# Kernel optimization log

Measured on AMD Instinct MI355X. Metric: run time of the kernel, lower is better.

Reference implementation:

```python
import jax, jax.numpy as jnp
import numpy as np

NC, K, SD = 8, 1024, 64
L = NC * SD
B = 8192
TAU = 0.07
COMMIT_W = 1.0
CONTRAST_W = 1.0
EPS = 1e-12


def setup_inputs() -> dict:
    key = jax.random.key(0)
    kz, ke = jax.random.split(key)
    z = jax.random.normal(kz, (B, L), dtype=jnp.float32)
    embeddings = jax.random.normal(ke, (NC, K, SD), dtype=jnp.float32)
    return {"z": z, "embeddings": embeddings}


def reference(z, embeddings):
    sg = jax.lax.stop_gradient
    Bn, Ln = z.shape
    nc, k, sd = embeddings.shape
    zr = z.reshape(Bn, nc, sd)  # (B, nc, sd)

    # squared distances via ||z||^2 - 2 z.e + ||e||^2 -> (B, nc, K), avoids (B,nc,K,sd)
    z2 = jnp.sum(zr * zr, axis=-1)[:, :, None]
    e2 = jnp.sum(embeddings * embeddings, axis=-1)[None, :, :]
    cross = jnp.einsum('bnd,nkd->bnk', zr, embeddings)
    dists = z2 - 2.0 * cross + e2
    indices = jnp.argmin(dists, axis=-1)  # (B, nc)

    # codebook gather
    quant_splits = embeddings[jnp.arange(nc)[None, :], indices]  # (B, nc, sd)
    quant_z = quant_splits.reshape(Bn, Ln)

    commit_loss = jnp.mean((sg(quant_z) - z) ** 2)
    embed_loss = jnp.mean((quant_z - sg(z)) ** 2)
    total_commit = commit_loss + embed_loss

    quant_z_st = z + sg(quant_z - z)

    z_norm = z / jnp.maximum(jnp.linalg.norm(z, axis=-1, keepdims=True), EPS)
    q_det = sg(quant_z)
    q_norm = q_det / jnp.maximum(jnp.linalg.norm(q_det, axis=-1, keepdims=True), EPS)
    logits = jnp.matmul(q_norm, z_norm.T) / TAU  # (B, B)
    # cross-entropy with labels = arange(B)
    contrastive = jnp.mean(jax.nn.logsumexp(logits, axis=1) - jnp.diagonal(logits))

    return (quant_z_st, COMMIT_W * total_commit, CONTRAST_W * contrastive, indices)
```

## Files before the change

kernel.cpp:

```cpp
#include <hip/hip_runtime.h>
#include <cstdint>
#include <cstddef>

#define NCB   8
#define KC    1024
#define SDIM  64
#define LDIM  512
#define BATCH 8192
#define INV_TAU (1.0f/0.07f)
#define K2E  20.60992915555662f
#define DBIAS 256.0f

typedef __bf16 bf16_t;
typedef bf16_t bf16x8 __attribute__((ext_vector_type(8)));
typedef float  floatx4 __attribute__((ext_vector_type(4)));
typedef int    intx8  __attribute__((ext_vector_type(8)));
typedef unsigned int u32;

__device__ __forceinline__ unsigned short f2bf(float f) {
    union { float f; unsigned int u; } c; c.f = f;
    unsigned int u = c.u;
    u += 0x7fffu + ((u >> 16) & 1u);
    return (unsigned short)(u >> 16);
}
__device__ __forceinline__ float bf2f(unsigned short h) {
    union { unsigned int u; float f; } c; c.u = ((unsigned int)h) << 16;
    return c.f;
}
__device__ __forceinline__ float exp2_fast(float x) {
    float r; asm("v_exp_f32 %0, %1" : "=v"(r) : "v"(x)); return r;
}
__device__ __forceinline__ void gll16(const void* g, void* l) {
    __builtin_amdgcn_global_load_lds(
        (const __attribute__((address_space(1))) u32*)g,
        (__attribute__((address_space(3))) u32*)l,
        16, 0, 0);
}

__global__ __launch_bounds__(256) void
k_pre(const float* __restrict__ emb, float* __restrict__ e2,
      unsigned short* __restrict__ eh, unsigned short* __restrict__ el,
      float* __restrict__ accs) {
    int gid = blockIdx.x * 256 + threadIdx.x;
    int row = gid >> 3, g = gid & 7;
    const float4* e4 = (const float4*)(emb + (size_t)row*SDIM + g*8);
    float4 a = e4[0], b = e4[1];
    union { ushort4 u4[2]; uint4 v; } H, L;
    H.u4[0].x=f2bf(a.x); L.u4[0].x=f2bf(a.x-bf2f(H.u4[0].x));
    H.u4[0].y=f2bf(a.y); L.u4[0].y=f2bf(a.y-bf2f(H.u4[0].y));
    H.u4[0].z=f2bf(a.z); L.u4[0].z=f2bf(a.z-bf2f(H.u4[0].z));
    H.u4[0].w=f2bf(a.w); L.u4[0].w=f2bf(a.w-bf2f(H.u4[0].w));
    H.u4[1].x=f2bf(b.x); L.u4[1].x=f2bf(b.x-bf2f(H.u4[1].x));
    H.u4[1].y=f2bf(b.y); L.u4[1].y=f2bf(b.y-bf2f(H.u4[1].y));
    H.u4[1].z=f2bf(b.z); L.u4[1].z=f2bf(b.z-bf2f(H.u4[1].z));
    H.u4[1].w=f2bf(b.w); L.u4[1].w=f2bf(b.w-bf2f(H.u4[1].w));
    *(uint4*)(eh + (size_t)row*SDIM + g*8) = H.v;
    *(uint4*)(el + (size_t)row*SDIM + g*8) = L.v;
    float s = a.x*a.x + a.y*a.y + a.z*a.z + a.w*a.w
            + b.x*b.x + b.y*b.y + b.z*b.z + b.w*b.w;
    s += __shfl_xor(s, 1); s += __shfl_xor(s, 2); s += __shfl_xor(s, 4);
    if (g == 0) e2[row] = s;
    if (gid == 0){ accs[0]=0.f; accs[1]=0.f; accs[2]=0.f; }
}

__device__ __forceinline__ double dist64d(const float* __restrict__ e,
                                          const float* __restrict__ zg) {
    double se=0.0, sz=0.0;
#pragma unroll 8
    for (int i=0;i<64;i++){ double ev=(double)e[i];
        se = fma(ev,ev,se); sz = fma(ev,(double)zg[i],sz); }
    return se - 2.0*sz;
}

__global__ __launch_bounds__(256,3) void
k_argmin(const unsigned short* __restrict__ eh, const unsigned short* __restrict__ el,
         const float* __restrict__ e2, const float* __restrict__ z,
         const float* __restrict__ emb, float* __restrict__ out_q,
         float* __restrict__ out_idx, float* __restrict__ accs) {
    __shared__ __align__(16) unsigned short Ah[128*64], Al[128*64];
    __shared__ __align__(16) unsigned short Bh[2][32*64], Bl[2][32*64];
    __shared__ float e2s[2][32];
    __shared__ unsigned int mK[2][128][2];

    const int tid = threadIdx.x;
    const int n   = blockIdx.y;
    const int i0  = blockIdx.x * 128;
    const int wid = tid >> 6, lane = tid & 63;
    const int wm = wid & 1, wn = wid >> 1;
    const int c  = lane & 15, qq = lane >> 4;

    const unsigned char* ehb = (const unsigned char*)(eh + (size_t)n*KC*SDIM);
    const unsigned char* elb = (const unsigned char*)(el + (size_t)n*KC*SDIM);
    const float* e2n = e2 + n*KC;

    const int brow = lane >> 3;
    const int bchk = ((lane & 7)*16) ^ (brow << 4);

    auto stageB = [&](int buf, int j0){
        int r0 = wid*8;
        size_t go = (size_t)(j0 + r0 + brow)*128 + bchk;
        gll16(ehb + go, &Bh[buf][r0*64]);
        gll16(elb + go, &Bl[buf][r0*64]);
    };

    stageB(0, 0);
    if (tid < 32) e2s[0][tid] = e2n[tid] + DBIAS;

#pragma unroll
    for (int s=0;s<8;s++){
        int seg = tid + s*256;
        int r = seg >> 4, sg = seg & 15;
        float4 v = *(const float4*)(z + (size_t)(i0+r)*LDIM + n*SDIM + sg*4);
        ushort4 h, l;
        h.x=f2bf(v.x); l.x=f2bf(v.x-bf2f(h.x));
        h.y=f2bf(v.y); l.y=f2bf(v.y-bf2f(h.y));
        h.z=f2bf(v.z); l.z=f2bf(v.z-bf2f(h.z));
        h.w=f2bf(v.w); l.w=f2bf(v.w-bf2f(h.w));
        int off = r*64 + ((sg*4) ^ ((r&7)<<3));
        *(ushort4*)(&Ah[off]) = h;
        *(ushort4*)(&Al[off]) = l;
    }

    unsigned int k1[16], k2[16];
#pragma unroll
    for (int j=0;j<16;j++){ k1[j]=0xFFFFFFFFu; k2[j]=0xFFFFFFFFu; }

    __syncthreads();

    for (int jt=0; jt<32; jt++){
        const int cur = jt & 1, nxt = cur ^ 1;
        const int j0 = jt*32;
        float e2r = 0.f;
        if (jt < 31){
            stageB(nxt, j0 + 32);
            if (tid < 32) e2r = e2n[j0 + 32 + tid];
        }

        floatx4 acc[4];
#pragma unroll
        for (int mt=0;mt<4;mt++) acc[mt] = (floatx4){0.f,0.f,0.f,0.f};

#pragma unroll
        for (int t=0;t<2;t++){
            const int axo = (t*32 + qq*8) ^ ((c&7)<<3);
            bf16x8 ah[4], alo[4], bh, bl;
            {
                int ro = (wn*16 + c)*64 + axo;
                bh = *(const bf16x8*)(&Bh[cur][ro]);
                bl = *(const bf16x8*)(&Bl[cur][ro]);
            }
#pragma unroll
            for (int mt=0;mt<4;mt++){
                int ro = (wm*64 + mt*16 + c)*64 + axo;
                ah[mt]  = *(const bf16x8*)(&Ah[ro]);
                alo[mt] = *(const bf16x8*)(&Al[ro]);
            }
#pragma unroll
            for (int mt=0;mt<4;mt++){
                acc[mt] = __builtin_amdgcn_mfma_f32_16x16x32_bf16(ah[mt],  bh, acc[mt], 0,0,0);
                acc[mt] = __builtin_amdgcn_mfma_f32_16x16x32_bf16(ah[mt],  bl, acc[mt], 0,0,0);
                acc[mt] = __builtin_amdgcn_mfma_f32_16x16x32_bf16(alo[mt], bh, acc[mt], 0,0,0);
            }
        }

        {
            const int colb = wn*16 + c;
            float e2v = e2s[cur][colb];
            unsigned int kidx = (unsigned int)(j0 + colb);
#pragma unroll
            for (int mt=0;mt<4;mt++)
#pragma unroll
                for (int reg=0;reg<4;reg++){
                    float d = fmaf(-2.0f, acc[mt][reg], e2v);
                    unsigned int key = (__float_as_uint(d) & 0xFFFFFC00u) | kidx;
                    int s = mt*4+reg;
                    unsigned int o1 = k1[s], o2 = k2[s];
                    unsigned int nk2;
                    asm("v_med3_u32 %0, %1, %2, %3" : "=v"(nk2) : "v"(o1), "v"(o2), "v"(key));
                    k2[s] = nk2;
                    k1[s] = min(o1, key);
                }
        }

        if (jt < 31 && tid < 32) e2s[nxt][tid] = e2r + DBIAS;
        __syncthreads();
    }

#pragma unroll
    for (int off=1; off<16; off<<=1){
#pragma unroll
        for (int s=0;s<16;s++){
            unsigned int o1 = __shfl_xor(k1[s], off);
            unsigned int o2 = __shfl_xor(k2[s], off);
            unsigned int n1 = min(k1[s], o1);
            k2[s] = min( max(k1[s], o1), min(k2[s], o2) );
            k1[s] = n1;
        }
    }
    if (c == 0){
#pragma unroll
        for (int s=0;s<16;s++){
            int row = wm*64 + (s>>2)*16 + qq*4 + (s&3);
            mK[wn][row][0] = k1[s]; mK[wn][row][1] = k2[s];
        }
    }
    __syncthreads();

    if (tid < 128){
        int b = i0 + tid;
        unsigned int a1 = mK[0][tid][0], a2 = mK[0][tid][1];
        unsigned int c1 = mK[1][tid][0], c2 = mK[1][tid][1];
        unsigned int f1 = min(a1, c1);
        unsigned int f2 = min( max(a1, c1), min(a2, c2) );
        int ii1 = (int)(f1 & 0x3FFu);
        int ii2 = (int)(f2 & 0x3FFu);
        float d1q = __uint_as_float(f1 & 0xFFFFFC00u);
        float d2q = __uint_as_float(f2 & 0xFFFFFC00u);

        const float* eb = emb + (size_t)n*KC*SDIM;
        const float* zg = z + (size_t)b*LDIM + n*SDIM;
        if (d2q - d1q < 0.08f) {
            double d1 = dist64d(eb + (size_t)ii1*SDIM, zg);
            double d2 = dist64d(eb + (size_t)ii2*SDIM, zg);
            if (d2 < d1 || (d2 == d1 && ii2 < ii1)) ii1 = ii2;
        }

        const float4* q4 = (const float4*)(eb + (size_t)ii1*SDIM);
        const float4* z4 = (const float4*)zg;
        float4* oq = (float4*)(out_q + (size_t)b*LDIM + n*SDIM);
        float cs = 0.f;
#pragma unroll
        for (int i=0;i<16;i++){
            float4 v = q4[i]; float4 zv = z4[i];
            oq[i] = v;
            float d0=v.x-zv.x, d1=v.y-zv.y, d2=v.z-zv.z, d3=v.w-zv.w;
            cs += d0*d0 + d1*d1 + d2*d2 + d3*d3;
        }
        out_idx[b*NCB + n] = (float)ii1;

        for (int off=32; off; off>>=1) cs += __shfl_down(cs, off);
        if ((tid & 63)==0) atomicAdd(&accs[0], cs);
    }
}

__global__ __launch_bounds__(256) void
k_norm(const float* __restrict__ z, const float* __restrict__ q,
       unsigned char* __restrict__ zn8, unsigned char* __restrict__ qn8,
       float* __restrict__ diag) {
    const int wid = threadIdx.x >> 6, lane = threadIdx.x & 63;
    const int b = blockIdx.x*4 + wid;
    const size_t base = (size_t)b*LDIM;
    const float4* z4 = (const float4*)(z + base + lane*8);
    const float4* q4 = (const float4*)(q + base + lane*8);
    float4 za = z4[0], zb = z4[1];
    float4 qa = q4[0], qb = q4[1];
    float sz = za.x*za.x + za.y*za.y + za.z*za.z + za.w*za.w
             + zb.x*zb.x + zb.y*zb.y + zb.z*zb.z + zb.w*zb.w;
    float sq = qa.x*qa.x + qa.y*qa.y + qa.z*qa.z + qa.w*qa.w
             + qb.x*qb.x + qb.y*qb.y + qb.z*qb.z + qb.w*qb.w;
    float sqz= qa.x*za.x + qa.y*za.y + qa.z*za.z + qa.w*za.w
             + qb.x*zb.x + qb.y*zb.y + qb.z*zb.z + qb.w*zb.w;
#pragma unroll
    for (int off=1; off<64; off<<=1){
        sz  += __shfl_xor(sz,  off);
        sq  += __shfl_xor(sq,  off);
        sqz += __shfl_xor(sqz, off);
    }
    float inz = 1.0f/fmaxf(sqrtf(sz), 1e-12f);
    float inq = 1.0f/fmaxf(sqrtf(sq), 1e-12f);
    if (lane == 0) diag[b] = sqz*inz*inq*INV_TAU;

    int z0 = __builtin_amdgcn_cvt_pk_fp8_f32(za.x*inz, za.y*inz, 0, false);
    z0     = __builtin_amdgcn_cvt_pk_fp8_f32(za.z*inz, za.w*inz, z0, true);
    int z1 = __builtin_amdgcn_cvt_pk_fp8_f32(zb.x*inz, zb.y*inz, 0, false);
    z1     = __builtin_amdgcn_cvt_pk_fp8_f32(zb.z*inz, zb.w*inz, z1, true);
    int q0 = __builtin_amdgcn_cvt_pk_fp8_f32(qa.x*inq, qa.y*inq, 0, false);
    q0     = __builtin_amdgcn_cvt_pk_fp8_f32(qa.z*inq, qa.w*inq, q0, true);
    int q1 = __builtin_amdgcn_cvt_pk_fp8_f32(qb.x*inq, qb.y*inq, 0, false);
    q1     = __builtin_amdgcn_cvt_pk_fp8_f32(qb.z*inq, qb.w*inq, q1, true);
    uint2 uz; uz.x = (unsigned)z0; uz.y = (unsigned)z1;
    uint2 uq; uq.x = (unsigned)q0; uq.y = (unsigned)q1;
    *(uint2*)(zn8 + base + lane*8) = uz;
    *(uint2*)(qn8 + base + lane*8) = uq;
}

__global__ __launch_bounds__(256,3) void
k_logits(const unsigned char* __restrict__ qn8, const unsigned char* __restrict__ zn8,
         float* __restrict__ Spart) {
    __shared__ __align__(16) unsigned char Bs[2][32*512];
    const int tid  = threadIdx.x;
    const int i0   = blockIdx.x * 128;
    const int chnk = blockIdx.y;
    const int wid  = tid >> 6, lane = tid & 63;
    const int wm = wid;
    const int c  = lane & 15, qq = lane >> 4;

    const int brow  = lane >> 5;
    const int bchk0 = (lane & 31) * 16;

    auto stageB = [&](int buf, int j0){
#pragma unroll
        for (int s=0;s<4;s++){
            int r0  = wid*8 + s*2;
            int row = r0 + brow;
            gll16(zn8 + (size_t)(j0+row)*LDIM + (bchk0 ^ ((row&7)<<4)),
                  &Bs[buf][r0*512]);
        }
    };

    stageB(0, chnk*1024);

    intx8 af[2][4];
#pragma unroll
    for (int mt=0;mt<2;mt++){
        const unsigned char* ap = qn8 + (size_t)(i0 + wm*32 + mt*16 + c)*LDIM + qq*32;
#pragma unroll
        for (int kc=0;kc<4;kc++){
            union { intx8 v; uint4 h[2]; } u;
            u.h[0] = *(const uint4*)(ap + kc*128);
            u.h[1] = *(const uint4*)(ap + kc*128 + 16);
            af[mt][kc] = u.v;
        }
    }
#pragma unroll
    for (int mt=0;mt<2;mt++)
#pragma unroll
        for (int kc=0;kc<4;kc++)
            asm volatile("" : "+v"(af[mt][kc]));

    float S[8];
#pragma unroll
    for (int i=0;i<8;i++) S[i] = 0.f;

    __syncthreads();

    for (int jt=0;jt<32;jt++){
        const int cur = jt & 1;
        const int j0 = chnk*1024 + jt*32;
        if (jt < 31) stageB(cur^1, j0 + 32);

        floatx4 acc[2][2];
#pragma unroll
        for (int mt=0;mt<2;mt++){
            acc[mt][0]=(floatx4){0.f,0.f,0.f,0.f};
            acc[mt][1]=(floatx4){0.f,0.f,0.f,0.f};
        }

#pragma unroll
        for (int kc=0;kc<4;kc++){
            intx8 bfr[2];
#pragma unroll
            for (int nt=0;nt<2;nt++){
                const int rb = nt*16 + c;
                const unsigned char* p = &Bs[cur][rb*512];
                const int o = kc*128 + qq*32;
                const int x = (rb&7)<<4;
                union { intx8 v; uint4 h[2]; } u;
                u.h[0] = *(const uint4*)(p + (o ^ x));
                u.h[1] = *(const uint4*)(p + ((o + 16) ^ x));
                bfr[nt] = u.v;
            }
#pragma unroll
            for (int mt=0;mt<2;mt++)
#pragma unroll
                for (int nt=0;nt<2;nt++)
                    acc[mt][nt] = __builtin_amdgcn_mfma_scale_f32_16x16x128_f8f6f4(
                        af[mt][kc], bfr[nt], acc[mt][nt],
                        0, 0,
                        0, 127,
                        0, 127);
        }

#pragma unroll
        for (int mt=0;mt<2;mt++)
#pragma unroll
            for (int reg=0;reg<4;reg++){
                float e0 = exp2_fast(fmaf(acc[mt][0][reg], K2E, -K2E));
                float e1 = exp2_fast(fmaf(acc[mt][1][reg], K2E, -K2E));
                S[mt*4+reg] += e0 + e1;
            }
        __syncthreads();
    }

#pragma unroll
    for (int off=1; off<16; off<<=1)
#pragma unroll
        for (int s=0;s<8;s++) S[s] += __shfl_xor(S[s], off);

    if (c == 0){
        const int p = chnk;
#pragma unroll
        for (int mt=0;mt<2;mt++)
#pragma unroll
            for (int reg=0;reg<4;reg++){
                int row = i0 + wm*32 + mt*16 + qq*4 + reg;
                Spart[p*BATCH + row] = S[mt*4+reg];
            }
    }
}

__global__ __launch_bounds__(256) void
k_finalize(const float* __restrict__ Spart, const float* __restrict__ diag,
           float* __restrict__ accs, float* __restrict__ out_s) {
    int r = blockIdx.x*256 + threadIdx.x;
    float Ssum = 0.f;
#pragma unroll
    for (int p=0;p<8;p++) Ssum += Spart[p*BATCH + r];
    float val = INV_TAU + logf(Ssum) - diag[r];
    for (int off=32; off; off>>=1) val += __shfl_down(val, off);
    if ((threadIdx.x & 63)==0) atomicAdd(&accs[1], val);
    __syncthreads();
    if (threadIdx.x == 0){
        __threadfence();
        unsigned int old = __float_as_uint(atomicAdd(&accs[2], 1.0f));
        if (old == __float_as_uint(31.0f)) {
            __threadfence();
            float a0 = atomicAdd(&accs[0], 0.0f);
            float a1 = atomicAdd(&accs[1], 0.0f);
            out_s[0] = 2.0f*a0 / (float)((size_t)BATCH*LDIM);
            out_s[1] = a1 / (float)BATCH;
        }
    }
}

extern "C" void kernel_launch(void* const* d_in, const int* in_sizes, int n_in,
                              void* d_out, int out_size, void* d_ws, size_t ws_size,
                              hipStream_t stream) {
    const float* z   = (const float*)d_in[0];
    const float* emb = (const float*)d_in[1];
    float* out = (float*)d_out;
    float* out_q       = out;
    float* out_scalars = out + 4194304;
    float* out_idx     = out + 4194306;

    float* wsf   = (float*)d_ws;
    float* e2    = wsf;
    float* accs  = wsf + 8192;
    float* diag  = wsf + 8704;
    float* Spart = wsf + 16896;
    unsigned char* qn8 = (unsigned char*)(Spart + 32*BATCH);
    unsigned char* zn8 = qn8 + (size_t)BATCH*LDIM;
    unsigned short* eh = (unsigned short*)(zn8 + (size_t)BATCH*LDIM);
    unsigned short* el = eh + (size_t)NCB*KC*SDIM;

    k_pre    <<<256,         256, 0, stream>>>(emb, e2, eh, el, accs);
    k_argmin <<<dim3(64,8),  256, 0, stream>>>(eh, el, e2, z, emb,
                                               out_q, out_idx, accs);
    k_norm   <<<2048,        256, 0, stream>>>(z, out_q, zn8, qn8, diag);
    k_logits <<<dim3(64,8),  256, 0, stream>>>(qn8, zn8, Spart);
    k_finalize<<<32,         256, 0, stream>>>(Spart, diag, accs, out_scalars);
}
```

Before: 171.5 us.

## Widen argmin codebook tile, split logits over more chunks, swizzle block mapping

k_argmin now stages 64 codebook rows per iteration instead of 32, so each wave computes two N-tiles and reuses its A fragments across twice the MFMAs. Launch bounds drop to 2 waves per SIMD to make room for the extra registers. k_logits splits the columns into 16 chunks of 512, doubling the grid to 1024 blocks with bounds raised to 4, and interleaves its B-fragment loads with the MFMAs. Both kernels remap block indices so neighbouring blocks share codebook or row data, which should help cache locality. Costs are higher register pressure and lower occupancy in argmin, plus more partial sums for finalize to reduce.

```diff
diff --git a/kernel.cpp b/kernel.cpp
--- a/kernel.cpp
+++ b/kernel.cpp
@@ -72,39 +72,22 @@
     return se - 2.0*sz;
 }
 
-__global__ __launch_bounds__(256,3) void
+__global__ __launch_bounds__(256,2) void
 k_argmin(const unsigned short* __restrict__ eh, const unsigned short* __restrict__ el,
          const float* __restrict__ e2, const float* __restrict__ z,
          const float* __restrict__ emb, float* __restrict__ out_q,
          float* __restrict__ out_idx, float* __restrict__ accs) {
     __shared__ __align__(16) unsigned short Ah[128*64], Al[128*64];
-    __shared__ __align__(16) unsigned short Bh[2][32*64], Bl[2][32*64];
-    __shared__ float e2s[2][32];
+    __shared__ __align__(16) unsigned short Bh[2][64*64], Bl[2][64*64];
+    __shared__ float e2s[2][64];
     __shared__ unsigned int mK[2][128][2];
 
     const int tid = threadIdx.x;
-    const int n   = blockIdx.y;
-    const int i0  = blockIdx.x * 128;
+    const int n   = blockIdx.x & 7;
+    const int i0  = (((blockIdx.x >> 3) << 3) + blockIdx.y) * 128;
     const int wid = tid >> 6, lane = tid & 63;
     const int wm = wid & 1, wn = wid >> 1;
     const int c  = lane & 15, qq = lane >> 4;
-
-    const unsigned char* ehb = (const unsigned char*)(eh + (size_t)n*KC*SDIM);
-    const unsigned char* elb = (const unsigned char*)(el + (size_t)n*KC*SDIM);
-    const float* e2n = e2 + n*KC;
-
-    const int brow = lane >> 3;
-    const int bchk = ((lane & 7)*16) ^ (brow << 4);
-
-    auto stageB = [&](int buf, int j0){
-        int r0 = wid*8;
-        size_t go = (size_t)(j0 + r0 + brow)*128 + bchk;
-        gll16(ehb + go, &Bh[buf][r0*64]);
-        gll16(elb + go, &Bl[buf][r0*64]);
-    };
-
-    stageB(0, 0);
-    if (tid < 32) e2s[0][tid] = e2n[tid] + DBIAS;
 
 #pragma unroll
     for (int s=0;s<8;s++){
@@ -121,34 +104,52 @@
         *(ushort4*)(&Al[off]) = l;
     }
 
+    const unsigned char* ehb = (const unsigned char*)(eh + (size_t)n*KC*SDIM);
+    const unsigned char* elb = (const unsigned char*)(el + (size_t)n*KC*SDIM);
+    const float* e2n = e2 + n*KC;
+
+    const int brow = lane >> 3;
+    const int bchk = ((lane & 7)*16) ^ (brow << 4);
+
+    auto stageB = [&](int buf, int j0){
+#pragma unroll
+        for (int s=0;s<2;s++){
+            int r0 = wid*16 + s*8;
+            size_t go = (size_t)(j0 + r0 + brow)*128 + bchk;
+            gll16(ehb + go, &Bh[buf][r0*64]);
+            gll16(elb + go, &Bl[buf][r0*64]);
+        }
+    };
+
+    if (tid < 64) e2s[0][tid] = e2n[tid] + DBIAS;
+    stageB(0, 0);
+
     unsigned int k1[16], k2[16];
 #pragma unroll
     for (int j=0;j<16;j++){ k1[j]=0xFFFFFFFFu; k2[j]=0xFFFFFFFFu; }
 
     __syncthreads();
 
-    for (int jt=0; jt<32; jt++){
+    for (int jt=0; jt<16; jt++){
         const int cur = jt & 1, nxt = cur ^ 1;
-        const int j0 = jt*32;
+        const int j0 = jt*64;
         float e2r = 0.f;
-        if (jt < 31){
-            stageB(nxt, j0 + 32);
-            if (tid < 32) e2r = e2n[j0 + 32 + tid];
-        }
-
-        floatx4 acc[4];
-#pragma unroll
-        for (int mt=0;mt<4;mt++) acc[mt] = (floatx4){0.f,0.f,0.f,0.f};
+        if (jt < 15){
+            stageB(nxt, j0 + 64);
+            if (tid < 64) e2r = e2n[j0 + 64 + tid];
+        }
+
+        floatx4 acc[4][2];
+#pragma unroll
+        for (int mt=0;mt<4;mt++){
+            acc[mt][0]=(floatx4){0.f,0.f,0.f,0.f};
+            acc[mt][1]=(floatx4){0.f,0.f,0.f,0.f};
+        }
 
 #pragma unroll
         for (int t=0;t<2;t++){
             const int axo = (t*32 + qq*8) ^ ((c&7)<<3);
-            bf16x8 ah[4], alo[4], bh, bl;
-            {
-                int ro = (wn*16 + c)*64 + axo;
-                bh = *(const bf16x8*)(&Bh[cur][ro]);
-                bl = *(const bf16x8*)(&Bl[cur][ro]);
-            }
+            bf16x8 ah[4], alo[4], bh[2], bl[2];
 #pragma unroll
             for (int mt=0;mt<4;mt++){
                 int ro = (wm*64 + mt*16 + c)*64 + axo;
@@ -156,22 +157,31 @@
                 alo[mt] = *(const bf16x8*)(&Al[ro]);
             }
 #pragma unroll
-            for (int mt=0;mt<4;mt++){
-                acc[mt] = __builtin_amdgcn_mfma_f32_16x16x32_bf16(ah[mt],  bh, acc[mt], 0,0,0);
-                acc[mt] = __builtin_amdgcn_mfma_f32_16x16x32_bf16(ah[mt],  bl, acc[mt], 0,0,0);
-                acc[mt] = __builtin_amdgcn_mfma_f32_16x16x32_bf16(alo[mt], bh, acc[mt], 0,0,0);
+            for (int nt=0;nt<2;nt++){
+                int ro = (wn*32 + nt*16 + c)*64 + axo;
+                bh[nt] = *(const bf16x8*)(&Bh[cur][ro]);
+                bl[nt] = *(const bf16x8*)(&Bl[cur][ro]);
             }
-        }
-
-        {
-            const int colb = wn*16 + c;
+#pragma unroll
+            for (int mt=0;mt<4;mt++)
+#pragma unroll
+                for (int nt=0;nt<2;nt++){
+                    acc[mt][nt] = __builtin_amdgcn_mfma_f32_16x16x32_bf16(ah[mt],  bh[nt], acc[mt][nt], 0,0,0);
+                    acc[mt][nt] = __builtin_amdgcn_mfma_f32_16x16x32_bf16(ah[mt],  bl[nt], acc[mt][nt], 0,0,0);
+                    acc[mt][nt] = __builtin_amdgcn_mfma_f32_16x16x32_bf16(alo[mt], bh[nt], acc[mt][nt], 0,0,0);
+                }
+        }
+
+#pragma unroll
+        for (int nt=0;nt<2;nt++){
+            const int colb = wn*32 + nt*16 + c;
             float e2v = e2s[cur][colb];
             unsigned int kidx = (unsigned int)(j0 + colb);
 #pragma unroll
             for (int mt=0;mt<4;mt++)
 #pragma unroll
                 for (int reg=0;reg<4;reg++){
-                    float d = fmaf(-2.0f, acc[mt][reg], e2v);
+                    float d = fmaf(-2.0f, acc[mt][nt][reg], e2v);
                     unsigned int key = (__float_as_uint(d) & 0xFFFFFC00u) | kidx;
                     int s = mt*4+reg;
                     unsigned int o1 = k1[s], o2 = k2[s];
@@ -182,7 +192,7 @@
                 }
         }
 
-        if (jt < 31 && tid < 32) e2s[nxt][tid] = e2r + DBIAS;
+        if (jt < 15 && tid < 64) e2s[nxt][tid] = e2r + DBIAS;
         __syncthreads();
     }
 
@@ -284,13 +294,13 @@
     *(uint2*)(qn8 + base + lane*8) = uq;
 }
 
-__global__ __launch_bounds__(256,3) void
+__global__ __launch_bounds__(256,4) void
 k_logits(const unsigned char* __restrict__ qn8, const unsigned char* __restrict__ zn8,
          float* __restrict__ Spart) {
     __shared__ __align__(16) unsigned char Bs[2][32*512];
     const int tid  = threadIdx.x;
-    const int i0   = blockIdx.x * 128;
-    const int chnk = blockIdx.y;
+    const int chnk = (blockIdx.x & 7) + ((blockIdx.y & 1) << 3);
+    const int i0   = (((blockIdx.x >> 3) << 3) + (blockIdx.y >> 1)) * 128;
     const int wid  = tid >> 6, lane = tid & 63;
     const int wm = wid;
     const int c  = lane & 15, qq = lane >> 4;
@@ -308,7 +318,7 @@
         }
     };
 
-    stageB(0, chnk*1024);
+    stageB(0, chnk*512);
 
     intx8 af[2][4];
 #pragma unroll
@@ -334,10 +344,10 @@
 
     __syncthreads();
 
-    for (int jt=0;jt<32;jt++){
+    for (int jt=0;jt<16;jt++){
         const int cur = jt & 1;
-        const int j0 = chnk*1024 + jt*32;
-        if (jt < 31) stageB(cur^1, j0 + 32);
+        const int j0 = chnk*512 + jt*32;
+        if (jt < 15) stageB(cur^1, j0 + 32);
 
         floatx4 acc[2][2];
 #pragma unroll
@@ -347,8 +357,7 @@
         }
 
 #pragma unroll
-        for (int kc=0;kc<4;kc++){
-            intx8 bfr[2];
+        for (int kc=0;kc<4;kc++)
 #pragma unroll
             for (int nt=0;nt<2;nt++){
                 const int rb = nt*16 + c;
@@ -358,18 +367,15 @@
                 union { intx8 v; uint4 h[2]; } u;
                 u.h[0] = *(const uint4*)(p + (o ^ x));
                 u.h[1] = *(const uint4*)(p + ((o + 16) ^ x));
-                bfr[nt] = u.v;
-            }
-#pragma unroll
-            for (int mt=0;mt<2;mt++)
-#pragma unroll
-                for (int nt=0;nt<2;nt++)
+                intx8 bfr = u.v;
+#pragma unroll
+                for (int mt=0;mt<2;mt++)
                     acc[mt][nt] = __builtin_amdgcn_mfma_scale_f32_16x16x128_f8f6f4(
-                        af[mt][kc], bfr[nt], acc[mt][nt],
+                        af[mt][kc], bfr, acc[mt][nt],
                         0, 0,
                         0, 127,
                         0, 127);
-        }
+            }
 
 #pragma unroll
         for (int mt=0;mt<2;mt++)
@@ -405,7 +411,7 @@
     int r = blockIdx.x*256 + threadIdx.x;
     float Ssum = 0.f;
 #pragma unroll
-    for (int p=0;p<8;p++) Ssum += Spart[p*BATCH + r];
+    for (int p=0;p<16;p++) Ssum += Spart[p*BATCH + r];
     float val = INV_TAU + logf(Ssum) - diag[r];
     for (int off=32; off; off>>=1) val += __shfl_down(val, off);
     if ((threadIdx.x & 63)==0) atomicAdd(&accs[1], val);
@@ -447,6 +453,6 @@
     k_argmin <<<dim3(64,8),  256, 0, stream>>>(eh, el, e2, z, emb,
                                                out_q, out_idx, accs);
     k_norm   <<<2048,        256, 0, stream>>>(z, out_q, zn8, qn8, diag);
-    k_logits <<<dim3(64,8),  256, 0, stream>>>(qn8, zn8, Spart);
+    k_logits <<<dim3(64,16), 256, 0, stream>>>(qn8, zn8, Spart);
     k_finalize<<<32,         256, 0, stream>>>(Spart, diag, accs, out_scalars);
 }
```

Measured after the change: 158.8 us. -7.4%, faster.

## Triple-buffer argmin and logits pipelines, split logits into more chunks, remap blocks

Applied to the files above, without the earlier changes.

Both the argmin and logits kernels move from double to triple buffering of the streamed operand. Each iteration now waits with an explicit vmcnt count followed by a raw s_barrier, so loads run two tiles ahead. The argmin kernel preloads all codebook norms into shared memory once and remaps block indices so blocks sharing a codebook run adjacently. The logits kernel halves its B tile, doubles the grid to 16 column chunks for more parallelism and occupancy, and raises launch bounds; finalize sums 16 partials. The risks are a lower occupancy hint for argmin and fragile manual waitcnt logic.

```diff
diff --git a/kernel.cpp b/kernel.cpp
--- a/kernel.cpp
+++ b/kernel.cpp
@@ -72,19 +72,19 @@
     return se - 2.0*sz;
 }
 
-__global__ __launch_bounds__(256,3) void
+__global__ __launch_bounds__(256,2) void
 k_argmin(const unsigned short* __restrict__ eh, const unsigned short* __restrict__ el,
          const float* __restrict__ e2, const float* __restrict__ z,
          const float* __restrict__ emb, float* __restrict__ out_q,
          float* __restrict__ out_idx, float* __restrict__ accs) {
     __shared__ __align__(16) unsigned short Ah[128*64], Al[128*64];
-    __shared__ __align__(16) unsigned short Bh[2][32*64], Bl[2][32*64];
-    __shared__ float e2s[2][32];
+    __shared__ __align__(16) unsigned short Bh[3][32*64], Bl[3][32*64];
+    __shared__ float e2s[1024];
     __shared__ unsigned int mK[2][128][2];
 
     const int tid = threadIdx.x;
-    const int n   = blockIdx.y;
-    const int i0  = blockIdx.x * 128;
+    const int n   = blockIdx.x & 7;
+    const int i0  = (((blockIdx.x >> 3) << 3) + blockIdx.y) * 128;
     const int wid = tid >> 6, lane = tid & 63;
     const int wm = wid & 1, wn = wid >> 1;
     const int c  = lane & 15, qq = lane >> 4;
@@ -104,7 +104,7 @@
     };
 
     stageB(0, 0);
-    if (tid < 32) e2s[0][tid] = e2n[tid] + DBIAS;
+    stageB(1, 32);
 
 #pragma unroll
     for (int s=0;s<8;s++){
@@ -120,6 +120,11 @@
         *(ushort4*)(&Ah[off]) = h;
         *(ushort4*)(&Al[off]) = l;
     }
+#pragma unroll
+    for (int s=0;s<4;s++){
+        int idx = tid + s*256;
+        e2s[idx] = e2n[idx] + DBIAS;
+    }
 
     unsigned int k1[16], k2[16];
 #pragma unroll
@@ -128,13 +133,9 @@
     __syncthreads();
 
     for (int jt=0; jt<32; jt++){
-        const int cur = jt & 1, nxt = cur ^ 1;
+        const int cur = jt % 3;
         const int j0 = jt*32;
-        float e2r = 0.f;
-        if (jt < 31){
-            stageB(nxt, j0 + 32);
-            if (tid < 32) e2r = e2n[j0 + 32 + tid];
-        }
+        if (jt < 30) stageB((jt+2)%3, j0 + 64);
 
         floatx4 acc[4];
 #pragma unroll
@@ -165,7 +166,7 @@
 
         {
             const int colb = wn*16 + c;
-            float e2v = e2s[cur][colb];
+            float e2v = e2s[j0 + colb];
             unsigned int kidx = (unsigned int)(j0 + colb);
 #pragma unroll
             for (int mt=0;mt<4;mt++)
@@ -182,8 +183,11 @@
                 }
         }
 
-        if (jt < 31 && tid < 32) e2s[nxt][tid] = e2r + DBIAS;
-        __syncthreads();
+        if (jt < 30) { asm volatile("s_waitcnt vmcnt(2)" ::: "memory"); }
+        else         { asm volatile("s_waitcnt vmcnt(0)" ::: "memory"); }
+        __builtin_amdgcn_sched_barrier(0);
+        __builtin_amdgcn_s_barrier();
+        __builtin_amdgcn_sched_barrier(0);
     }
 
 #pragma unroll
@@ -284,13 +288,13 @@
     *(uint2*)(qn8 + base + lane*8) = uq;
 }
 
-__global__ __launch_bounds__(256,3) void
+__global__ __launch_bounds__(256,4) void
 k_logits(const unsigned char* __restrict__ qn8, const unsigned char* __restrict__ zn8,
          float* __restrict__ Spart) {
-    __shared__ __align__(16) unsigned char Bs[2][32*512];
+    __shared__ __align__(16) unsigned char Bs[3][16*512];
     const int tid  = threadIdx.x;
-    const int i0   = blockIdx.x * 128;
-    const int chnk = blockIdx.y;
+    const int chnk = (blockIdx.x & 7) + ((blockIdx.y & 1) << 3);
+    const int i0   = (((blockIdx.x >> 3) << 3) + (blockIdx.y >> 1)) * 128;
     const int wid  = tid >> 6, lane = tid & 63;
     const int wm = wid;
     const int c  = lane & 15, qq = lane >> 4;
@@ -300,15 +304,17 @@
 
     auto stageB = [&](int buf, int j0){
 #pragma unroll
-        for (int s=0;s<4;s++){
-            int r0  = wid*8 + s*2;
+        for (int s=0;s<2;s++){
+            int r0  = wid*4 + s*2;
             int row = r0 + brow;
             gll16(zn8 + (size_t)(j0+row)*LDIM + (bchk0 ^ ((row&7)<<4)),
                   &Bs[buf][r0*512]);
         }
     };
 
-    stageB(0, chnk*1024);
+    const int c0 = chnk*512;
+    stageB(0, c0);
+    stageB(1, c0 + 16);
 
     intx8 af[2][4];
 #pragma unroll
@@ -335,51 +341,43 @@
     __syncthreads();
 
     for (int jt=0;jt<32;jt++){
-        const int cur = jt & 1;
-        const int j0 = chnk*1024 + jt*32;
-        if (jt < 31) stageB(cur^1, j0 + 32);
-
-        floatx4 acc[2][2];
-#pragma unroll
-        for (int mt=0;mt<2;mt++){
-            acc[mt][0]=(floatx4){0.f,0.f,0.f,0.f};
-            acc[mt][1]=(floatx4){0.f,0.f,0.f,0.f};
-        }
+        const int cur = jt % 3;
+        const int j0 = c0 + jt*16;
+        if (jt < 30) stageB((jt+2)%3, j0 + 32);
+
+        floatx4 acc[2];
+        acc[0]=(floatx4){0.f,0.f,0.f,0.f};
+        acc[1]=(floatx4){0.f,0.f,0.f,0.f};
 
 #pragma unroll
         for (int kc=0;kc<4;kc++){
-            intx8 bfr[2];
-#pragma unroll
-            for (int nt=0;nt<2;nt++){
-                const int rb = nt*16 + c;
-                const unsigned char* p = &Bs[cur][rb*512];
-                const int o = kc*128 + qq*32;
-                const int x = (rb&7)<<4;
-                union { intx8 v; uint4 h[2]; } u;
-                u.h[0] = *(const uint4*)(p + (o ^ x));
-                u.h[1] = *(const uint4*)(p + ((o + 16) ^ x));
-                bfr[nt] = u.v;
-            }
+            const unsigned char* p = &Bs[cur][c*512];
+            const int o = kc*128 + qq*32;
+            const int x = (c&7)<<4;
+            union { intx8 v; uint4 h[2]; } u;
+            u.h[0] = *(const uint4*)(p + (o ^ x));
+            u.h[1] = *(const uint4*)(p + ((o + 16) ^ x));
+            intx8 bfr = u.v;
 #pragma unroll
             for (int mt=0;mt<2;mt++)
-#pragma unroll
-                for (int nt=0;nt<2;nt++)
-                    acc[mt][nt] = __builtin_amdgcn_mfma_scale_f32_16x16x128_f8f6f4(
-                        af[mt][kc], bfr[nt], acc[mt][nt],
-                        0, 0,
-                        0, 127,
-                        0, 127);
+                acc[mt] = __builtin_amdgcn_mfma_scale_f32_16x16x128_f8f6f4(
+                    af[mt][kc], bfr, acc[mt],
+                    0, 0,
+                    0, 127,
+                    0, 127);
         }
 
 #pragma unroll
         for (int mt=0;mt<2;mt++)
 #pragma unroll
-            for (int reg=0;reg<4;reg++){
-                float e0 = exp2_fast(fmaf(acc[mt][0][reg], K2E, -K2E));
-                float e1 = exp2_fast(fmaf(acc[mt][1][reg], K2E, -K2E));
-                S[mt*4+reg] += e0 + e1;
-            }
-        __syncthreads();
+            for (int reg=0;reg<4;reg++)
+                S[mt*4+reg] += exp2_fast(fmaf(acc[mt][reg], K2E, -K2E));
+
+        if (jt < 30) { asm volatile("s_waitcnt vmcnt(2)" ::: "memory"); }
+        else         { asm volatile("s_waitcnt vmcnt(0)" ::: "memory"); }
+        __builtin_amdgcn_sched_barrier(0);
+        __builtin_amdgcn_s_barrier();
+        __builtin_amdgcn_sched_barrier(0);
     }
 
 #pragma unroll
@@ -405,7 +403,7 @@
     int r = blockIdx.x*256 + threadIdx.x;
     float Ssum = 0.f;
 #pragma unroll
-    for (int p=0;p<8;p++) Ssum += Spart[p*BATCH + r];
+    for (int p=0;p<16;p++) Ssum += Spart[p*BATCH + r];
     float val = INV_TAU + logf(Ssum) - diag[r];
     for (int off=32; off; off>>=1) val += __shfl_down(val, off);
     if ((threadIdx.x & 63)==0) atomicAdd(&accs[1], val);
@@ -447,6 +445,6 @@
     k_argmin <<<dim3(64,8),  256, 0, stream>>>(eh, el, e2, z, emb,
                                                out_q, out_idx, accs);
     k_norm   <<<2048,        256, 0, stream>>>(z, out_q, zn8, qn8, diag);
-    k_logits <<<dim3(64,8),  256, 0, stream>>>(qn8, zn8, Spart);
+    k_logits <<<dim3(64,16), 256, 0, stream>>>(qn8, zn8, Spart);
     k_finalize<<<32,         256, 0, stream>>>(Spart, diag, accs, out_scalars);
 }
```

New measurement: 170.2 us. Within noise of the previous version (-0.7%).
